# Kernel optimization log

Hardware: AMD Instinct MI355X
Metric: run time of the kernel (lower is better)

## Reference

```python
import jax, jax.numpy as jnp
import numpy as np
from jax import lax

# dims
BATCH, SEQ, DMODEL = 2, 2048, 1024
EXPAND, HEADDIM, DSTATE, DCONV, MLP_INNER = 2, 64, 64, 4, 4096
DIN = EXPAND * DMODEL            # 2048
NH = DIN // HEADDIM              # 32 heads
CONV_DIM = DIN + 2 * DSTATE      # x, B, C go through the depthwise conv
DPROJ = 2 * DIN + 2 * DSTATE + NH  # z, xBC, dt
EPS = 1e-5


def rmsnorm(x, w):
    return x * lax.rsqrt(jnp.mean(x * x, axis=-1, keepdims=True) + EPS) * w


def setup_inputs() -> dict:
    key = jax.random.key(0)
    ks = jax.random.split(key, 12)
    n = lambda i, shape, scale: jax.random.normal(ks[i], shape, jnp.float32) * scale
    return {
        "hidden_tokens": n(0, (BATCH, SEQ, DMODEL), 1.0),
        "W_in": n(1, (DMODEL, DPROJ), DMODEL ** -0.5),
        "conv_w": n(2, (CONV_DIM, DCONV), 0.2),
        "conv_b": jnp.zeros((CONV_DIM,), jnp.float32),
        "dt_bias": jax.random.uniform(ks[3], (NH,), jnp.float32, -4.0, -1.0),
        "A_log": jnp.log(jax.random.uniform(ks[4], (NH,), jnp.float32, 1.0, 16.0)),
        "D_param": n(5, (NH,), 1.0),
        "norm_w": jnp.ones((DIN,), jnp.float32),
        "W_out": n(6, (DIN, DMODEL), DIN ** -0.5),
        "rms_w": jnp.ones((DMODEL,), jnp.float32),
        "mlp_w1": n(7, (DMODEL, MLP_INNER), DMODEL ** -0.5),
        "mlp_b1": jnp.zeros((MLP_INNER,), jnp.float32),
        "mlp_w2": n(8, (MLP_INNER, DMODEL), MLP_INNER ** -0.5),
        "mlp_b2": jnp.zeros((DMODEL,), jnp.float32),
    }


def _mamba2(x, W_in, conv_w, conv_b, dt_bias, A_log, D_param, norm_w, W_out):
    b, l, _ = x.shape
    zxbcdt = x @ W_in                                   # (b,l,DPROJ)
    z = zxbcdt[..., :DIN]
    xBC = zxbcdt[..., DIN:DIN + CONV_DIM]
    dt = zxbcdt[..., DIN + CONV_DIM:]                   # (b,l,NH)

    # depthwise causal conv1d over sequence
    xt = jnp.pad(xBC, ((0, 0), (DCONV - 1, 0), (0, 0))).transpose(0, 2, 1)  # (b,c,l+pad)
    conv = lax.conv_general_dilated(xt, conv_w[:, None, :], (1,), "VALID",
                                    feature_group_count=CONV_DIM,
                                    dimension_numbers=("NCH", "OIH", "NCH"))
    xBC = jax.nn.silu(conv.transpose(0, 2, 1) + conv_b)  # (b,l,CONV_DIM)

    xs = xBC[..., :DIN].reshape(b, l, NH, HEADDIM)       # (b,l,h,p)
    Bc = xBC[..., DIN:DIN + DSTATE]                      # (b,l,n), ngroups=1
    Cc = xBC[..., DIN + DSTATE:]                         # (b,l,n)

    dt = jax.nn.softplus(dt + dt_bias)                   # (b,l,h)
    A = -jnp.exp(A_log)                                  # (h,)
    dA = jnp.exp(dt * A)                                 # (b,l,h)
    dtx = dt[..., None] * xs                             # (b,l,h,p)

    def step(h, inp):
        dA_t, dtx_t, B_t, C_t = inp                      # (b,h),(b,h,p),(b,n),(b,n)
        h = dA_t[..., None, None] * h + dtx_t[..., None] * B_t[:, None, None, :]
        y = jnp.einsum("bhpn,bn->bhp", h, C_t)
        return h, y

    h0 = jnp.zeros((b, NH, HEADDIM, DSTATE), x.dtype)
    _, ys = lax.scan(step, h0, (dA.transpose(1, 0, 2), dtx.transpose(1, 0, 2, 3),
                                Bc.transpose(1, 0, 2), Cc.transpose(1, 0, 2)))
    y = ys.transpose(1, 0, 2, 3) + D_param[None, None, :, None] * xs  # (b,l,h,p)
    y = y.reshape(b, l, DIN)
    y = rmsnorm(y * jax.nn.silu(z), norm_w)              # gated RMSNorm
    return y @ W_out


def reference(hidden_tokens, W_in, conv_w, conv_b, dt_bias, A_log, D_param,
              norm_w, W_out, rms_w, mlp_w1, mlp_b1, mlp_w2, mlp_b2):
    h = hidden_tokens + _mamba2(hidden_tokens, W_in, conv_w, conv_b, dt_bias,
                                A_log, D_param, norm_w, W_out)
    hn = rmsnorm(h, rms_w)
    mlp = jax.nn.silu(hn @ mlp_w1 + mlp_b1) @ mlp_w2 + mlp_b2
    return h + mlp
```

## Files before the change

### kernel.cpp

```cpp
#include <hip/hip_runtime.h>
#include <hip/hip_bf16.h>
#include <cstdint>
#include <cstddef>

#define BATCH 2
#define SEQ 2048
#define DMODEL 1024
#define DIN 2048
#define NH 32
#define HEADDIM 64
#define DSTATE 64
#define DCONV 4
#define CONV_DIM (DIN + 2 * DSTATE)
#define DPROJ (2 * DIN + 2 * DSTATE + NH)
#define MLP_INNER 4096
#define TOKENS (BATCH * SEQ)
#define EPS 1e-5f
#define Q 64
#define NCHUNK (SEQ / Q)
#define NCH (BATCH * NCHUNK * NH)
#define LSTR 72
#define NPAD_IN 4352

typedef __attribute__((ext_vector_type(8))) short short8;
typedef __attribute__((ext_vector_type(8))) __bf16 bf16x8;
typedef __attribute__((ext_vector_type(4))) float f32x4;

__device__ inline short f2bf(float f) {
    unsigned u = __builtin_bit_cast(unsigned, f);
    u = (u + 0x7FFFu + ((u >> 16) & 1u)) >> 16;
    return (short)u;
}
__device__ inline float bf2f(short s) {
    unsigned u = ((unsigned)(unsigned short)s) << 16;
    return __builtin_bit_cast(float, u);
}
__device__ inline float silu_f(float x) { return x / (1.f + __expf(-x)); }

__device__ inline bf16x8 ld_frag(const short* p) {
    short8 s = *(const short8*)p;
    return __builtin_bit_cast(bf16x8, s);
}

__device__ inline void glds16(const short* g, short* l) {
    __builtin_amdgcn_global_load_lds(
        (const __attribute__((address_space(1))) void*)g,
        (__attribute__((address_space(3))) void*)l, 16, 0, 0);
}

template <int MODE, int KT>
__global__ __launch_bounds__(256, (KT == 32) ? 4 : 2) void gemm_bf16_kernel(
    const short* __restrict__ A, const short* __restrict__ BT,
    void* __restrict__ Cout, const float* __restrict__ bias,
    const float* __restrict__ res, int M, int N, int K)
{
    const int tid  = threadIdx.x;
    const int wid  = tid >> 6;
    const int lane = tid & 63;
    const int lm   = lane & 15;
    const int lg   = lane >> 4;

    const int nb  = gridDim.x * gridDim.y;
    const int bid = blockIdx.y * gridDim.x + blockIdx.x;
    const int per = nb >> 3;
    const int nid = (bid & 7) * per + (bid >> 3);
    const int m0  = (nid / gridDim.x) * 128;
    const int n0  = (nid % gridDim.x) * 128;

    __shared__ __attribute__((aligned(16))) short Al0[128 * KT];
    __shared__ __attribute__((aligned(16))) short Al1[128 * KT];
    __shared__ __attribute__((aligned(16))) short Bl0[128 * KT];
    __shared__ __attribute__((aligned(16))) short Bl1[128 * KT];

    f32x4 acc[4][4];
#pragma unroll
    for (int i = 0; i < 4; ++i)
#pragma unroll
        for (int j = 0; j < 4; ++j) acc[i][j] = {0.f, 0.f, 0.f, 0.f};

    const int wm = (wid >> 1) * 64;
    const int wn = (wid & 1) * 64;

    constexpr int lpr = KT / 8;
    constexpr int rpi = 64 / lpr;
    constexpr int nin = 32 / rpi;
    const int srow = lane / lpr;
    const int scb  = (lane % lpr) ^ (srow & (lpr - 1));
    const int scol = scb * 8;
    const short* Ag = A  + (size_t)(m0 + wid * 32 + srow) * K + scol;
    const short* Bg = BT + (size_t)(n0 + wid * 32 + srow) * K + scol;
    const int woff = wid * 32 * KT;

    const int niter = K / KT;
    {
#pragma unroll
        for (int j = 0; j < nin; ++j) {
            glds16(Ag + (size_t)j * rpi * K, Al0 + woff + j * 512);
            glds16(Bg + (size_t)j * rpi * K, Bl0 + woff + j * 512);
        }
    }

    for (int i = 0; i < niter; ++i) {
        __syncthreads();
        const short* Ac = (i & 1) ? Al1 : Al0;
        const short* Bc = (i & 1) ? Bl1 : Bl0;
        if (i + 1 < niter) {
            int kt = (i + 1) * KT;
            short* al = ((i & 1) ? Al0 : Al1) + woff;
            short* bl = ((i & 1) ? Bl0 : Bl1) + woff;
#pragma unroll
            for (int j = 0; j < nin; ++j) {
                glds16(Ag + kt + (size_t)j * rpi * K, al + j * 512);
                glds16(Bg + kt + (size_t)j * rpi * K, bl + j * 512);
            }
        }

#pragma unroll
        for (int sub = 0; sub < KT / 32; ++sub) {
            const int cb = sub * 4 + lg;
            bf16x8 af[4], bf[4];
#pragma unroll
            for (int ii = 0; ii < 4; ++ii) {
                int ar = wm + ii * 16 + lm;
                af[ii] = ld_frag(&Ac[ar * KT + ((cb ^ (ar & (lpr - 1))) * 8)]);
            }
#pragma unroll
            for (int j = 0; j < 4; ++j) {
                int br = wn + j * 16 + lm;
                bf[j] = ld_frag(&Bc[br * KT + ((cb ^ (br & (lpr - 1))) * 8)]);
            }
#pragma unroll
            for (int ii = 0; ii < 4; ++ii)
#pragma unroll
                for (int j = 0; j < 4; ++j)
                    acc[ii][j] = __builtin_amdgcn_mfma_f32_16x16x32_bf16(af[ii], bf[j], acc[ii][j], 0, 0, 0);
        }
    }

#pragma unroll
    for (int i = 0; i < 4; ++i) {
#pragma unroll
        for (int j = 0; j < 4; ++j) {
            int col = n0 + wn + j * 16 + lm;
            if (col >= N) continue;
            float bv = (MODE == 1 || MODE == 2) ? bias[col] : 0.f;
#pragma unroll
            for (int r = 0; r < 4; ++r) {
                int row = m0 + wm + i * 16 + lg * 4 + r;
                float v = acc[i][j][r];
                if (MODE == 1) {
                    ((short*)Cout)[(size_t)row * N + col] = f2bf(silu_f(v + bv));
                } else if (MODE == 4) {
                    ((short*)Cout)[(size_t)row * N + col] = f2bf(v);
                } else {
                    if (MODE == 2) v = v + bv + res[(size_t)row * N + col];
                    if (MODE == 3) v = v + res[(size_t)row * N + col];
                    ((float*)Cout)[(size_t)row * N + col] = v;
                }
            }
        }
    }
}

__global__ __launch_bounds__(256) void cvt_kernel(
    const float* __restrict__ src, short* __restrict__ dst, int n4)
{
    int i = (blockIdx.x * 256 + threadIdx.x);
    if (i >= n4) return;
    f32x4 v = *(const f32x4*)(src + (size_t)i * 4);
    short4 o;
    o.x = f2bf(v.x); o.y = f2bf(v.y); o.z = f2bf(v.z); o.w = f2bf(v.w);
    *(short4*)(dst + (size_t)i * 4) = o;
}

__global__ __launch_bounds__(256) void transpose_kernel(
    const float* __restrict__ src, short* __restrict__ dst, int K, int N)
{
    __shared__ float t[32][33];
    int bx = blockIdx.x, by = blockIdx.y;
    int col = threadIdx.x & 31, row8 = threadIdx.x >> 5;
    int gn = bx * 32 + col;
#pragma unroll
    for (int r = 0; r < 4; ++r) {
        int gk = by * 32 + row8 + r * 8;
        t[row8 + r * 8][col] = (gn < N) ? src[(size_t)gk * N + gn] : 0.f;
    }
    __syncthreads();
#pragma unroll
    for (int r = 0; r < 4; ++r) {
        int n = bx * 32 + row8 + r * 8;
        dst[(size_t)n * K + by * 32 + col] = f2bf(t[col][row8 + r * 8]);
    }
}

#define CTOK 8
__global__ __launch_bounds__(256) void conv_kernel(
    const short* __restrict__ zx, const float* __restrict__ cw,
    const float* __restrict__ cb, short* __restrict__ xBCc)
{
    int c4 = blockIdx.y * 256 + threadIdx.x;
    if (c4 >= CONV_DIM / 4) return;
    int c  = c4 * 4;
    int m0 = blockIdx.x * CTOK;
    int l0 = m0 & (SEQ - 1);

    const short* base = zx + (size_t)m0 * DPROJ + DIN + c;
    f32x4 win[CTOK + 3];
#pragma unroll
    for (int j = 0; j < CTOK + 3; ++j) {
        int off = j - 3;
        if (l0 + off >= 0) {
            short4 sv = *(const short4*)(base + (ptrdiff_t)off * DPROJ);
            win[j] = {bf2f(sv.x), bf2f(sv.y), bf2f(sv.z), bf2f(sv.w)};
        } else {
            win[j] = {0.f, 0.f, 0.f, 0.f};
        }
    }
    f32x4 w0 = *(const f32x4*)(cw + (c + 0) * DCONV);
    f32x4 w1 = *(const f32x4*)(cw + (c + 1) * DCONV);
    f32x4 w2 = *(const f32x4*)(cw + (c + 2) * DCONV);
    f32x4 w3 = *(const f32x4*)(cw + (c + 3) * DCONV);
    f32x4 bb = *(const f32x4*)(cb + c);

    short* outp = xBCc + (size_t)m0 * CONV_DIM + c;
#pragma unroll
    for (int t = 0; t < CTOK; ++t) {
        f32x4 a = {bb.x, bb.y, bb.z, bb.w};
#pragma unroll
        for (int j = 0; j < DCONV; ++j) {
            f32x4 v = win[t + j];
            a.x += v.x * w0[j];
            a.y += v.y * w1[j];
            a.z += v.z * w2[j];
            a.w += v.w * w3[j];
        }
        short4 o;
        o.x = f2bf(silu_f(a.x)); o.y = f2bf(silu_f(a.y));
        o.z = f2bf(silu_f(a.z)); o.w = f2bf(silu_f(a.w));
        *(short4*)(outp + (size_t)t * CONV_DIM) = o;
    }
}

__global__ __launch_bounds__(256) void dt_kernel(
    const short* __restrict__ zx, const float* __restrict__ dt_bias,
    const float* __restrict__ A_log, float* __restrict__ dtb, float* __restrict__ ldab)
{
    int idx = blockIdx.x * 256 + threadIdx.x;
    if (idx >= TOKENS * NH) return;
    int hh = idx & (NH - 1);
    int m  = idx >> 5;
    float v  = bf2f(zx[(size_t)m * DPROJ + DIN + CONV_DIM + hh]) + dt_bias[hh];
    float dt = (v > 20.f) ? v : log1pf(__expf(v));
    dtb[idx]  = dt;
    ldab[idx] = -__expf(A_log[hh]) * dt;
}

__global__ __launch_bounds__(256) void chunk_kernel(
    const short* __restrict__ xBCc, const float* __restrict__ dtb,
    const float* __restrict__ ldab, float* __restrict__ ybuf,
    float* __restrict__ Sbuf, float* __restrict__ cumdecay)
{
    int bid = blockIdx.x;
    int h = bid & 31, c = (bid >> 5) & 31, b = bid >> 10;
    int m0 = b * SEQ + c * Q;
    int tid = threadIdx.x;
    int wid = tid >> 6, lane = tid & 63, lm = lane & 15, lg = lane >> 4;

    __shared__ __attribute__((aligned(16))) short Cc[64 * LSTR];
    __shared__ __attribute__((aligned(16))) short Bb[64 * LSTR];
    __shared__ __attribute__((aligned(16))) short BwT[64 * LSTR];
    __shared__ __attribute__((aligned(16))) short Xt[64 * LSTR];
    __shared__ __attribute__((aligned(16))) short Mm[64 * LSTR];
    __shared__ float Lc[64], dtv[64];

    if (tid < 64) {
        int s = tid;
        size_t ix = (size_t)(m0 + s) * NH + h;
        float ld = ldab[ix];
        float dt = dtb[ix];
        float v = ld;
#pragma unroll
        for (int off = 1; off < 64; off <<= 1) {
            float o = __shfl_up(v, off);
            if (s >= off) v += o;
        }
        Lc[s] = v;
        dtv[s] = dt;
        cumdecay[(size_t)bid * 64 + s] = __expf(v);
    }
    {
        int row = tid >> 2, c0 = (tid & 3) * 16;
        const short* pB = xBCc + (size_t)(m0 + row) * CONV_DIM + DIN;
#pragma unroll
        for (int u = 0; u < 2; ++u) {
            short8 vb = *(const short8*)(pB + c0 + 8 * u);
            short8 vc = *(const short8*)(pB + DSTATE + c0 + 8 * u);
            *(short8*)&Bb[row * LSTR + c0 + 8 * u] = vb;
            *(short8*)&Cc[row * LSTR + c0 + 8 * u] = vc;
        }
    }
    __syncthreads();
    {
        int s = tid >> 2, c0 = (tid & 3) * 16;
        float w = dtv[s];
        float w2 = __expf(Lc[63] - Lc[s]);
        const short* pX = xBCc + (size_t)(m0 + s) * CONV_DIM + h * HEADDIM;
#pragma unroll
        for (int u = 0; u < 4; ++u) {
            short4 v = *(const short4*)(pX + c0 + 4 * u);
            Xt[(c0 + 4 * u + 0) * LSTR + s] = f2bf(bf2f(v.x) * w);
            Xt[(c0 + 4 * u + 1) * LSTR + s] = f2bf(bf2f(v.y) * w);
            Xt[(c0 + 4 * u + 2) * LSTR + s] = f2bf(bf2f(v.z) * w);
            Xt[(c0 + 4 * u + 3) * LSTR + s] = f2bf(bf2f(v.w) * w);
            short4 sb = *(short4*)&Bb[s * LSTR + c0 + 4 * u];
            BwT[(c0 + 4 * u + 0) * LSTR + s] = f2bf(bf2f(sb.x) * w2);
            BwT[(c0 + 4 * u + 1) * LSTR + s] = f2bf(bf2f(sb.y) * w2);
            BwT[(c0 + 4 * u + 2) * LSTR + s] = f2bf(bf2f(sb.z) * w2);
            BwT[(c0 + 4 * u + 3) * LSTR + s] = f2bf(bf2f(sb.w) * w2);
        }
    }
    __syncthreads();

    {
        bf16x8 af[2];
#pragma unroll
        for (int kk = 0; kk < 2; ++kk)
            af[kk] = ld_frag(&Cc[(wid * 16 + lm) * LSTR + kk * 32 + lg * 8]);
#pragma unroll
        for (int j = 0; j < 4; ++j) {
            f32x4 acc = {0.f, 0.f, 0.f, 0.f};
#pragma unroll
            for (int kk = 0; kk < 2; ++kk) {
                bf16x8 bf = ld_frag(&Bb[(j * 16 + lm) * LSTR + kk * 32 + lg * 8]);
                acc = __builtin_amdgcn_mfma_f32_16x16x32_bf16(af[kk], bf, acc, 0, 0, 0);
            }
            int s = j * 16 + lm;
            float Ls = Lc[s];
#pragma unroll
            for (int r = 0; r < 4; ++r) {
                int t = wid * 16 + lg * 4 + r;
                float val = (s <= t) ? acc[r] * __expf(Lc[t] - Ls) : 0.f;
                Mm[t * LSTR + s] = f2bf(val);
            }
        }
    }
    __syncthreads();

    {
        bf16x8 am[2], aw[2];
#pragma unroll
        for (int kk = 0; kk < 2; ++kk) {
            am[kk] = ld_frag(&Mm[(wid * 16 + lm) * LSTR + kk * 32 + lg * 8]);
            aw[kk] = ld_frag(&BwT[(wid * 16 + lm) * LSTR + kk * 32 + lg * 8]);
        }
#pragma unroll
        for (int j = 0; j < 4; ++j) {
            f32x4 a1 = {0.f, 0.f, 0.f, 0.f};
            f32x4 a2 = {0.f, 0.f, 0.f, 0.f};
#pragma unroll
            for (int kk = 0; kk < 2; ++kk) {
                bf16x8 bx = ld_frag(&Xt[(j * 16 + lm) * LSTR + kk * 32 + lg * 8]);
                a1 = __builtin_amdgcn_mfma_f32_16x16x32_bf16(am[kk], bx, a1, 0, 0, 0);
                a2 = __builtin_amdgcn_mfma_f32_16x16x32_bf16(aw[kk], bx, a2, 0, 0, 0);
            }
            int p = j * 16 + lm;
#pragma unroll
            for (int r = 0; r < 4; ++r) {
                int t = wid * 16 + lg * 4 + r;
                ybuf[(size_t)(m0 + t) * DIN + h * HEADDIM + p] = a1[r];
                Sbuf[(size_t)bid * 4096 + t * 64 + p] = a2[r];
            }
        }
    }
}

__global__ __launch_bounds__(256) void state_kernel(
    float* __restrict__ SH, const float* __restrict__ cumdecay)
{
    int bh = blockIdx.x;
    int b = bh >> 5, h = bh & 31;
    int tid = threadIdx.x;
    f32x4 H[4];
#pragma unroll
    for (int u = 0; u < 4; ++u) H[u] = {0.f, 0.f, 0.f, 0.f};
    for (int c = 0; c < NCHUNK; ++c) {
        int cid = (b * NCHUNK + c) * NH + h;
        size_t base = (size_t)cid * 4096 + (size_t)tid * 16;
        float cd = cumdecay[(size_t)cid * 64 + 63];
        f32x4 s[4];
#pragma unroll
        for (int u = 0; u < 4; ++u) s[u] = *(const f32x4*)(SH + base + u * 4);
#pragma unroll
        for (int u = 0; u < 4; ++u) *(f32x4*)(SH + base + u * 4) = H[u];
#pragma unroll
        for (int u = 0; u < 4; ++u) {
            H[u].x = cd * H[u].x + s[u].x;
            H[u].y = cd * H[u].y + s[u].y;
            H[u].z = cd * H[u].z + s[u].z;
            H[u].w = cd * H[u].w + s[u].w;
        }
    }
}

__global__ __launch_bounds__(256) void inter_kernel(
    const short* __restrict__ xBCc, const float* __restrict__ Hin,
    const float* __restrict__ cumdecay, float* __restrict__ ybuf)
{
    int bid = blockIdx.x;
    int h = bid & 31, c = (bid >> 5) & 31, b = bid >> 10;
    int m0 = b * SEQ + c * Q;
    int tid = threadIdx.x;
    int wid = tid >> 6, lane = tid & 63, lm = lane & 15, lg = lane >> 4;

    __shared__ __attribute__((aligned(16))) short Cc[64 * LSTR];
    __shared__ __attribute__((aligned(16))) short HT[64 * LSTR];
    __shared__ float eLc[64];

    if (tid < 64) eLc[tid] = cumdecay[(size_t)bid * 64 + tid];
    {
        int row = tid >> 2, c0 = (tid & 3) * 16;
        const short* pC = xBCc + (size_t)(m0 + row) * CONV_DIM + DIN + DSTATE;
#pragma unroll
        for (int u = 0; u < 2; ++u) {
            short8 vc = *(const short8*)(pC + c0 + 8 * u);
            *(short8*)&Cc[row * LSTR + c0 + 8 * u] = vc;
        }
        const float* pH = Hin + (size_t)bid * 4096 + row * 64;
#pragma unroll
        for (int u = 0; u < 4; ++u) {
            f32x4 vh = *(const f32x4*)(pH + c0 + 4 * u);
            HT[(c0 + 4 * u + 0) * LSTR + row] = f2bf(vh.x);
            HT[(c0 + 4 * u + 1) * LSTR + row] = f2bf(vh.y);
            HT[(c0 + 4 * u + 2) * LSTR + row] = f2bf(vh.z);
            HT[(c0 + 4 * u + 3) * LSTR + row] = f2bf(vh.w);
        }
    }
    __syncthreads();

    bf16x8 af[2];
#pragma unroll
    for (int kk = 0; kk < 2; ++kk)
        af[kk] = ld_frag(&Cc[(wid * 16 + lm) * LSTR + kk * 32 + lg * 8]);
#pragma unroll
    for (int j = 0; j < 4; ++j) {
        f32x4 acc = {0.f, 0.f, 0.f, 0.f};
#pragma unroll
        for (int kk = 0; kk < 2; ++kk) {
            bf16x8 bh_ = ld_frag(&HT[(j * 16 + lm) * LSTR + kk * 32 + lg * 8]);
            acc = __builtin_amdgcn_mfma_f32_16x16x32_bf16(af[kk], bh_, acc, 0, 0, 0);
        }
        int p = j * 16 + lm;
#pragma unroll
        for (int r = 0; r < 4; ++r) {
            int t = wid * 16 + lg * 4 + r;
            size_t ya = (size_t)(m0 + t) * DIN + h * HEADDIM + p;
            ybuf[ya] += eLc[t] * acc[r];
        }
    }
}

__global__ __launch_bounds__(256) void norm1_kernel(
    const short* __restrict__ zx, const short* __restrict__ xBCc,
    const float* __restrict__ Dp, const float* __restrict__ y,
    short* __restrict__ ybf, const float* __restrict__ w)
{
    int m = blockIdx.x;
    int t = threadIdx.x;
    const short* zr = zx + (size_t)m * DPROJ;
    const short* xr = xBCc + (size_t)m * CONV_DIM;
    const float* yr = y + (size_t)m * DIN;
    float vals[8];
    float ss = 0.f;
#pragma unroll
    for (int j = 0; j < 8; ++j) {
        int i = j * 256 + t;
        float v = (yr[i] + Dp[i >> 6] * bf2f(xr[i])) * silu_f(bf2f(zr[i]));
        vals[j] = v;
        ss += v * v;
    }
#pragma unroll
    for (int o = 32; o >= 1; o >>= 1) ss += __shfl_xor(ss, o);
    __shared__ float wsum[4];
    if ((t & 63) == 0) wsum[t >> 6] = ss;
    __syncthreads();
    float tot = wsum[0] + wsum[1] + wsum[2] + wsum[3];
    float scale = rsqrtf(tot / (float)DIN + EPS);
#pragma unroll
    for (int j = 0; j < 8; ++j) {
        int i = j * 256 + t;
        ybf[(size_t)m * DIN + i] = f2bf(vals[j] * scale * w[i]);
    }
}

__global__ __launch_bounds__(256) void norm2_kernel(
    const float* __restrict__ hb, short* __restrict__ hnbf, const float* __restrict__ w)
{
    int m = blockIdx.x;
    int t = threadIdx.x;
    const float* hr = hb + (size_t)m * DMODEL;
    float vals[4];
    float ss = 0.f;
#pragma unroll
    for (int j = 0; j < 4; ++j) {
        int i = j * 256 + t;
        float v = hr[i];
        vals[j] = v;
        ss += v * v;
    }
#pragma unroll
    for (int o = 32; o >= 1; o >>= 1) ss += __shfl_xor(ss, o);
    __shared__ float wsum[4];
    if ((t & 63) == 0) wsum[t >> 6] = ss;
    __syncthreads();
    float tot = wsum[0] + wsum[1] + wsum[2] + wsum[3];
    float scale = rsqrtf(tot / (float)DMODEL + EPS);
#pragma unroll
    for (int j = 0; j < 4; ++j) {
        int i = j * 256 + t;
        hnbf[(size_t)m * DMODEL + i] = f2bf(vals[j] * scale * w[i]);
    }
}

extern "C" void kernel_launch(void* const* d_in, const int* in_sizes, int n_in,
                              void* d_out, int out_size, void* d_ws, size_t ws_size,
                              hipStream_t stream) {
    const float* x       = (const float*)d_in[0];
    const float* W_in    = (const float*)d_in[1];
    const float* conv_w  = (const float*)d_in[2];
    const float* conv_b  = (const float*)d_in[3];
    const float* dt_bias = (const float*)d_in[4];
    const float* A_log   = (const float*)d_in[5];
    const float* D_param = (const float*)d_in[6];
    const float* norm_w  = (const float*)d_in[7];
    const float* W_out   = (const float*)d_in[8];
    const float* rms_w   = (const float*)d_in[9];
    const float* mlp_w1  = (const float*)d_in[10];
    const float* mlp_b1  = (const float*)d_in[11];
    const float* mlp_w2  = (const float*)d_in[12];
    const float* mlp_b2  = (const float*)d_in[13];
    float* out = (float*)d_out;

    float* ws       = (float*)d_ws;
    float* zxf      = ws;
    float* xBCf     = zxf + (size_t)TOKENS * DPROJ;
    float* dtb      = xBCf + (size_t)TOKENS * CONV_DIM;
    float* ldab     = dtb + (size_t)TOKENS * NH;
    float* cumdecay = ldab + (size_t)TOKENS * NH;
    float* ybuf     = cumdecay + (size_t)TOKENS * NH;
    float* SH       = ybuf + (size_t)TOKENS * DIN;
    float* bfarea   = SH + (size_t)NCH * 4096;

    short* zxb   = (short*)zxf;
    short* xBCb  = (short*)xBCf;
    short* xbf   = (short*)ybuf;
    short* midbf = (short*)ybuf;
    float* hbuf  = SH;
    short* hnbf  = (short*)(SH + (size_t)TOKENS * DMODEL);

    short* ybf   = (short*)bfarea;
    short* WinT  = ybf + (size_t)TOKENS * DIN;
    short* WoutT = WinT + (size_t)NPAD_IN * DMODEL;
    short* w1T   = WoutT + (size_t)DMODEL * DIN;
    short* w2T   = w1T + (size_t)MLP_INNER * DMODEL;

    dim3 blk(256);

    cvt_kernel<<<dim3(TOKENS * DMODEL / 4 / 256), blk, 0, stream>>>(x, xbf, TOKENS * DMODEL / 4);
    transpose_kernel<<<dim3(NPAD_IN / 32, DMODEL / 32), blk, 0, stream>>>(W_in, WinT, DMODEL, DPROJ);
    transpose_kernel<<<dim3(DMODEL / 32, DIN / 32), blk, 0, stream>>>(W_out, WoutT, DIN, DMODEL);
    transpose_kernel<<<dim3(MLP_INNER / 32, DMODEL / 32), blk, 0, stream>>>(mlp_w1, w1T, DMODEL, MLP_INNER);
    transpose_kernel<<<dim3(DMODEL / 32, MLP_INNER / 32), blk, 0, stream>>>(mlp_w2, w2T, MLP_INNER, DMODEL);

    gemm_bf16_kernel<4, 32><<<dim3(NPAD_IN / 128, TOKENS / 128), blk, 0, stream>>>(
        xbf, WinT, zxb, nullptr, nullptr, TOKENS, DPROJ, DMODEL);
    conv_kernel<<<dim3(TOKENS / CTOK, (CONV_DIM / 4 + 255) / 256), blk, 0, stream>>>(
        zxb, conv_w, conv_b, xBCb);
    dt_kernel<<<dim3(TOKENS * NH / 256), blk, 0, stream>>>(zxb, dt_bias, A_log, dtb, ldab);
    chunk_kernel<<<dim3(NCH), blk, 0, stream>>>(xBCb, dtb, ldab, ybuf, SH, cumdecay);
    state_kernel<<<dim3(BATCH * NH), blk, 0, stream>>>(SH, cumdecay);
    inter_kernel<<<dim3(NCH), blk, 0, stream>>>(xBCb, SH, cumdecay, ybuf);
    norm1_kernel<<<dim3(TOKENS), blk, 0, stream>>>(zxb, xBCb, D_param, ybuf, ybf, norm_w);
    gemm_bf16_kernel<3, 64><<<dim3(DMODEL / 128, TOKENS / 128), blk, 0, stream>>>(
        ybf, WoutT, hbuf, nullptr, x, TOKENS, DMODEL, DIN);
    norm2_kernel<<<dim3(TOKENS), blk, 0, stream>>>(hbuf, hnbf, rms_w);
    gemm_bf16_kernel<1, 32><<<dim3(MLP_INNER / 128, TOKENS / 128), blk, 0, stream>>>(
        hnbf, w1T, midbf, mlp_b1, nullptr, TOKENS, MLP_INNER, DMODEL);
    gemm_bf16_kernel<2, 64><<<dim3(DMODEL / 128, TOKENS / 128), blk, 0, stream>>>(
        midbf, w2T, out, mlp_b2, hbuf, TOKENS, DMODEL, MLP_INNER);
}
```

Baseline: 424.9 us.

## Add 64-row GEMM for narrow outputs, split state scan, vectorize norms

Adds a 64x128-tile bf16 GEMM with double-buffered LDS, XOR swizzle and XCD-aware block remapping. It replaces the 128x128 kernel for the two N=1024 output projections, raising the block count from 256 to 512 so more CUs are busy. The state scan now splits each head's state across 4 blocks and prefetches the next chunk, adding parallelism to a serial kernel. Both RMSNorm kernels switch to contiguous vector loads and stores per thread.

```diff
diff --git a/kernel.cpp b/kernel.cpp
--- a/kernel.cpp
+++ b/kernel.cpp
@@ -162,6 +162,109 @@
     }
 }
 
+template <int MODE>
+__global__ __launch_bounds__(256, 2) void gemm64_kernel(
+    const short* __restrict__ A, const short* __restrict__ BT,
+    float* __restrict__ Cout, const float* __restrict__ bias,
+    const float* __restrict__ res, int M, int N, int K)
+{
+    constexpr int KT = 64;
+    const int tid  = threadIdx.x;
+    const int wid  = tid >> 6;
+    const int lane = tid & 63;
+    const int lm   = lane & 15;
+    const int lg   = lane >> 4;
+    const int wn   = wid * 32;
+
+    const int nb  = gridDim.x * gridDim.y;
+    const int bid = blockIdx.y * gridDim.x + blockIdx.x;
+    const int per = nb >> 3;
+    const int nid = (bid & 7) * per + (bid >> 3);
+    const int m0  = (nid / gridDim.x) * 64;
+    const int n0  = (nid % gridDim.x) * 128;
+
+    __shared__ __attribute__((aligned(16))) short Al0[64 * KT];
+    __shared__ __attribute__((aligned(16))) short Al1[64 * KT];
+    __shared__ __attribute__((aligned(16))) short Bl0[128 * KT];
+    __shared__ __attribute__((aligned(16))) short Bl1[128 * KT];
+
+    f32x4 acc[4][2];
+#pragma unroll
+    for (int i = 0; i < 4; ++i)
+#pragma unroll
+        for (int j = 0; j < 2; ++j) acc[i][j] = {0.f, 0.f, 0.f, 0.f};
+
+    const int srow = lane >> 3;
+    const int scb  = (lane & 7) ^ (srow & 7);
+    const int scol = scb * 8;
+    const short* Bg = BT + (size_t)(n0 + wid * 32 + srow) * K + scol;
+    const short* Ag = A  + (size_t)(m0 + (wid & 1) * 32 + srow) * K + scol;
+    const int woffB = wid * 32 * KT;
+    const int woffA = (wid & 1) * 32 * KT;
+    const bool doA = (wid < 2);
+
+    const int niter = K / KT;
+    {
+#pragma unroll
+        for (int j = 0; j < 4; ++j) {
+            if (doA) glds16(Ag + (size_t)j * 8 * K, Al0 + woffA + j * 512);
+            glds16(Bg + (size_t)j * 8 * K, Bl0 + woffB + j * 512);
+        }
+    }
+
+    for (int i = 0; i < niter; ++i) {
+        __syncthreads();
+        const short* Ac = (i & 1) ? Al1 : Al0;
+        const short* Bc = (i & 1) ? Bl1 : Bl0;
+        if (i + 1 < niter) {
+            int kt = (i + 1) * KT;
+            short* al = ((i & 1) ? Al0 : Al1) + woffA;
+            short* bl = ((i & 1) ? Bl0 : Bl1) + woffB;
+#pragma unroll
+            for (int j = 0; j < 4; ++j) {
+                if (doA) glds16(Ag + kt + (size_t)j * 8 * K, al + j * 512);
+                glds16(Bg + kt + (size_t)j * 8 * K, bl + j * 512);
+            }
+        }
+
+#pragma unroll
+        for (int sub = 0; sub < 2; ++sub) {
+            const int cb = sub * 4 + lg;
+            bf16x8 af[4], bf[2];
+#pragma unroll
+            for (int ii = 0; ii < 4; ++ii) {
+                int ar = ii * 16 + lm;
+                af[ii] = ld_frag(&Ac[ar * KT + ((cb ^ (ar & 7)) * 8)]);
+            }
+#pragma unroll
+            for (int j = 0; j < 2; ++j) {
+                int br = wn + j * 16 + lm;
+                bf[j] = ld_frag(&Bc[br * KT + ((cb ^ (br & 7)) * 8)]);
+            }
+#pragma unroll
+            for (int ii = 0; ii < 4; ++ii)
+#pragma unroll
+                for (int j = 0; j < 2; ++j)
+                    acc[ii][j] = __builtin_amdgcn_mfma_f32_16x16x32_bf16(af[ii], bf[j], acc[ii][j], 0, 0, 0);
+        }
+    }
+
+#pragma unroll
+    for (int j = 0; j < 2; ++j) {
+        int col = n0 + wn + j * 16 + lm;
+        float bv = (MODE == 2) ? bias[col] : 0.f;
+#pragma unroll
+        for (int i = 0; i < 4; ++i) {
+#pragma unroll
+            for (int r = 0; r < 4; ++r) {
+                int row = m0 + i * 16 + lg * 4 + r;
+                float v = acc[i][j][r] + bv + res[(size_t)row * N + col];
+                Cout[(size_t)row * N + col] = v;
+            }
+        }
+    }
+}
+
 __global__ __launch_bounds__(256) void cvt_kernel(
     const float* __restrict__ src, short* __restrict__ dst, int n4)
 {
@@ -377,28 +480,30 @@
 __global__ __launch_bounds__(256) void state_kernel(
     float* __restrict__ SH, const float* __restrict__ cumdecay)
 {
-    int bh = blockIdx.x;
+    int bh = blockIdx.x >> 2, st = blockIdx.x & 3;
     int b = bh >> 5, h = bh & 31;
-    int tid = threadIdx.x;
-    f32x4 H[4];
-#pragma unroll
-    for (int u = 0; u < 4; ++u) H[u] = {0.f, 0.f, 0.f, 0.f};
+    size_t off = (size_t)st * 1024 + (size_t)threadIdx.x * 4;
+
+    f32x4 H = {0.f, 0.f, 0.f, 0.f};
+    int cid = b * NCHUNK * NH + h;
+    f32x4 s_next = *(const f32x4*)(SH + (size_t)cid * 4096 + off);
+    float cd_next = cumdecay[(size_t)cid * 64 + 63];
+
     for (int c = 0; c < NCHUNK; ++c) {
-        int cid = (b * NCHUNK + c) * NH + h;
-        size_t base = (size_t)cid * 4096 + (size_t)tid * 16;
-        float cd = cumdecay[(size_t)cid * 64 + 63];
-        f32x4 s[4];
-#pragma unroll
-        for (int u = 0; u < 4; ++u) s[u] = *(const f32x4*)(SH + base + u * 4);
-#pragma unroll
-        for (int u = 0; u < 4; ++u) *(f32x4*)(SH + base + u * 4) = H[u];
-#pragma unroll
-        for (int u = 0; u < 4; ++u) {
-            H[u].x = cd * H[u].x + s[u].x;
-            H[u].y = cd * H[u].y + s[u].y;
-            H[u].z = cd * H[u].z + s[u].z;
-            H[u].w = cd * H[u].w + s[u].w;
-        }
+        f32x4 s = s_next;
+        float cd = cd_next;
+        size_t base = (size_t)cid * 4096 + off;
+        if (c + 1 < NCHUNK) {
+            int cid1 = cid + NH;
+            s_next = *(const f32x4*)(SH + (size_t)cid1 * 4096 + off);
+            cd_next = cumdecay[(size_t)cid1 * 64 + 63];
+        }
+        *(f32x4*)(SH + base) = H;
+        H.x = cd * H.x + s.x;
+        H.y = cd * H.y + s.y;
+        H.z = cd * H.z + s.z;
+        H.w = cd * H.w + s.w;
+        cid += NH;
     }
 }
 
@@ -466,15 +571,20 @@
 {
     int m = blockIdx.x;
     int t = threadIdx.x;
-    const short* zr = zx + (size_t)m * DPROJ;
-    const short* xr = xBCc + (size_t)m * CONV_DIM;
-    const float* yr = y + (size_t)m * DIN;
+    int i0 = t * 8;
+    const short8 zv = *(const short8*)(zx + (size_t)m * DPROJ + i0);
+    const short8 xv = *(const short8*)(xBCc + (size_t)m * CONV_DIM + i0);
+    const float* yr = y + (size_t)m * DIN + i0;
+    f32x4 y0 = *(const f32x4*)(yr);
+    f32x4 y1 = *(const f32x4*)(yr + 4);
+    float Dv = Dp[i0 >> 6];
+
     float vals[8];
     float ss = 0.f;
 #pragma unroll
     for (int j = 0; j < 8; ++j) {
-        int i = j * 256 + t;
-        float v = (yr[i] + Dp[i >> 6] * bf2f(xr[i])) * silu_f(bf2f(zr[i]));
+        float yj = (j < 4) ? y0[j] : y1[j - 4];
+        float v = (yj + Dv * bf2f(xv[j])) * silu_f(bf2f(zv[j]));
         vals[j] = v;
         ss += v * v;
     }
@@ -485,11 +595,16 @@
     __syncthreads();
     float tot = wsum[0] + wsum[1] + wsum[2] + wsum[3];
     float scale = rsqrtf(tot / (float)DIN + EPS);
+
+    f32x4 w0 = *(const f32x4*)(w + i0);
+    f32x4 w1 = *(const f32x4*)(w + i0 + 4);
+    short8 ov;
 #pragma unroll
     for (int j = 0; j < 8; ++j) {
-        int i = j * 256 + t;
-        ybf[(size_t)m * DIN + i] = f2bf(vals[j] * scale * w[i]);
-    }
+        float wj = (j < 4) ? w0[j] : w1[j - 4];
+        ov[j] = f2bf(vals[j] * scale * wj);
+    }
+    *(short8*)(ybf + (size_t)m * DIN + i0) = ov;
 }
 
 __global__ __launch_bounds__(256) void norm2_kernel(
@@ -497,16 +612,9 @@
 {
     int m = blockIdx.x;
     int t = threadIdx.x;
-    const float* hr = hb + (size_t)m * DMODEL;
-    float vals[4];
-    float ss = 0.f;
-#pragma unroll
-    for (int j = 0; j < 4; ++j) {
-        int i = j * 256 + t;
-        float v = hr[i];
-        vals[j] = v;
-        ss += v * v;
-    }
+    int i0 = t * 4;
+    f32x4 hv = *(const f32x4*)(hb + (size_t)m * DMODEL + i0);
+    float ss = hv.x * hv.x + hv.y * hv.y + hv.z * hv.z + hv.w * hv.w;
 #pragma unroll
     for (int o = 32; o >= 1; o >>= 1) ss += __shfl_xor(ss, o);
     __shared__ float wsum[4];
@@ -514,11 +622,13 @@
     __syncthreads();
     float tot = wsum[0] + wsum[1] + wsum[2] + wsum[3];
     float scale = rsqrtf(tot / (float)DMODEL + EPS);
-#pragma unroll
-    for (int j = 0; j < 4; ++j) {
-        int i = j * 256 + t;
-        hnbf[(size_t)m * DMODEL + i] = f2bf(vals[j] * scale * w[i]);
-    }
+    f32x4 wv = *(const f32x4*)(w + i0);
+    short4 ov;
+    ov.x = f2bf(hv.x * scale * wv.x);
+    ov.y = f2bf(hv.y * scale * wv.y);
+    ov.z = f2bf(hv.z * scale * wv.z);
+    ov.w = f2bf(hv.w * scale * wv.w);
+    *(short4*)(hnbf + (size_t)m * DMODEL + i0) = ov;
 }
 
 extern "C" void kernel_launch(void* const* d_in, const int* in_sizes, int n_in,
@@ -577,14 +687,14 @@
         zxb, conv_w, conv_b, xBCb);
     dt_kernel<<<dim3(TOKENS * NH / 256), blk, 0, stream>>>(zxb, dt_bias, A_log, dtb, ldab);
     chunk_kernel<<<dim3(NCH), blk, 0, stream>>>(xBCb, dtb, ldab, ybuf, SH, cumdecay);
-    state_kernel<<<dim3(BATCH * NH), blk, 0, stream>>>(SH, cumdecay);
+    state_kernel<<<dim3(BATCH * NH * 4), blk, 0, stream>>>(SH, cumdecay);
     inter_kernel<<<dim3(NCH), blk, 0, stream>>>(xBCb, SH, cumdecay, ybuf);
     norm1_kernel<<<dim3(TOKENS), blk, 0, stream>>>(zxb, xBCb, D_param, ybuf, ybf, norm_w);
-    gemm_bf16_kernel<3, 64><<<dim3(DMODEL / 128, TOKENS / 128), blk, 0, stream>>>(
+    gemm64_kernel<3><<<dim3(DMODEL / 128, TOKENS / 64), blk, 0, stream>>>(
         ybf, WoutT, hbuf, nullptr, x, TOKENS, DMODEL, DIN);
     norm2_kernel<<<dim3(TOKENS), blk, 0, stream>>>(hbuf, hnbf, rms_w);
     gemm_bf16_kernel<1, 32><<<dim3(MLP_INNER / 128, TOKENS / 128), blk, 0, stream>>>(
         hnbf, w1T, midbf, mlp_b1, nullptr, TOKENS, MLP_INNER, DMODEL);
-    gemm_bf16_kernel<2, 64><<<dim3(DMODEL / 128, TOKENS / 128), blk, 0, stream>>>(
+    gemm64_kernel<2><<<dim3(DMODEL / 128, TOKENS / 64), blk, 0, stream>>>(
         midbf, w2T, out, mlp_b2, hbuf, TOKENS, DMODEL, MLP_INNER);
 }
```

After: 412.8 us. -2.9%, faster.
